# Performance work log

Hardware: AMD Instinct MI355X
Metric: run time of the kernel (lower is better)

The kernel has to match this reference:

```python
import jax, jax.numpy as jnp
import numpy as np

B, L, H, D = 4096, 256, 32, 2
LOG_PROB_FACTOR = 0.5

def setup_inputs() -> dict:
    key = jax.random.key(0)
    k0, k1, k2, k3 = jax.random.split(key, 4)
    x = jax.random.randint(k0, (B, L), 0, D)  # spin configs in {0,1}
    Wi = jax.random.normal(k1, (D, 4 * H), dtype=jnp.float32) * 0.1   # input kernel (no bias, flax LSTMCell)
    Wh = jax.random.normal(k2, (H, 4 * H), dtype=jnp.float32) * 0.1   # recurrent kernel
    bh = jnp.zeros((4 * H,), dtype=jnp.float32)                        # recurrent bias
    Wo = jax.random.normal(k3, (H, D), dtype=jnp.float32) * 0.1       # output Dense kernel
    bo = jnp.zeros((D,), dtype=jnp.float32)                            # output Dense bias
    return {"x": x, "Wi": Wi, "Wh": Wh, "bh": bh, "Wo": Wo, "bo": bo}

def reference(x, Wi, Wh, bh, Wo, bo):
    # one-hot of spin t-1 (zeros at t=0); log-prob is read out at spin t.
    x_oh = jax.nn.one_hot(x, D, dtype=Wi.dtype)      # [B, L, D]
    xs = jnp.swapaxes(x_oh, 0, 1)                    # [L, B, D] time-major for scan
    c0 = jnp.zeros((x.shape[0], H), Wi.dtype)
    h0 = jnp.zeros((x.shape[0], H), Wi.dtype)
    inp0 = jnp.zeros((x.shape[0], D), Wi.dtype)      # jnp.zeros(inputDim) initial input

    def step(carry, xt):
        c, h, inp = carry
        gates = inp @ Wi + h @ Wh + bh               # [B, 4H]
        i, f, g, o = jnp.split(gates, 4, axis=-1)    # flax LSTMCell gate order i,f,g,o
        c_new = jax.nn.sigmoid(f) * c + jax.nn.sigmoid(i) * jnp.tanh(g)
        h_new = jax.nn.sigmoid(o) * jnp.tanh(c_new)
        out = jax.nn.elu(h_new @ Wo + bo)            # Dense + actFun, [B, D]
        # log(sum(softmax(out) * onehot)) == gathered log_softmax (stable form)
        logp = jnp.sum(jax.nn.log_softmax(out, axis=-1) * xt, axis=-1)  # [B]
        return (c_new, h_new, xt), logp

    _, logps = jax.lax.scan(step, (c0, h0, inp0), xs)  # logps: [L, B]
    return LOG_PROB_FACTOR * jnp.sum(logps, axis=0)    # [B]
```

## Files before the change

kernel.cpp:

```cpp
#include <hip/hip_runtime.h>


typedef __attribute__((ext_vector_type(8))) short bf16x8;
typedef __attribute__((ext_vector_type(4))) float f32x4;

#define LOG2E 1.4426950408889634f
#define LN2   0.6931471805599453f

__device__ __forceinline__ float fexp2(float x) { return __builtin_amdgcn_exp2f(x); }
__device__ __forceinline__ float flog2(float x) { return __builtin_amdgcn_logf(x); }
__device__ __forceinline__ float frcp(float x)  { return __builtin_amdgcn_rcpf(x); }

__device__ __forceinline__ float fsig(float x)   { return frcp(1.f + fexp2(-LOG2E * x)); }
__device__ __forceinline__ float ftanh_(float x) { return 1.f - 2.f * frcp(fexp2(2.f * LOG2E * x) + 1.f); }
__device__ __forceinline__ float felu(float x)   { return x > 0.f ? x : fexp2(LOG2E * x) - 1.f; }

__device__ __forceinline__ unsigned short f2bf(float f) {
    unsigned u = __builtin_bit_cast(unsigned, f);
    u = (u + 0x7FFFu + ((u >> 16) & 1u)) >> 16;
    return (unsigned short)u;
}

constexpr int Bsz = 4096;

__global__ __launch_bounds__(512, 2) void lstm_r10(
    const int*   __restrict__ x,
    const float* __restrict__ Wi,
    const float* __restrict__ Wh,
    const float* __restrict__ bh,
    const float* __restrict__ Wo,
    const float* __restrict__ bo,
    float*       __restrict__ out)
{
    const int tid  = threadIdx.x;
    const int w    = tid >> 6;
    const int lane = tid & 63;
    const int m    = lane & 15;
    const int oct  = lane >> 4;
    const int rot  = w & 3;
    const int half = w >> 2;
    const int b0   = blockIdx.x * 16;

    __shared__ char   spinT[16][260];
    __shared__ float2 Sbuf[256][16];
    __shared__ short  hbuf[2][16][40];
    __shared__ float  red[8][16];

    {
        const int bl = tid >> 5;
        const int c8 = (tid & 31) * 8;
        const int4* src = reinterpret_cast<const int4*>(x + (b0 + bl) * 256 + c8);
        const int4 v0 = src[0], v1 = src[1];
        const int p0 = (v0.x & 1) | ((v0.y & 1) << 8) | ((v0.z & 1) << 16) | ((v0.w & 1) << 24);
        const int p1 = (v1.x & 1) | ((v1.y & 1) << 8) | ((v1.z & 1) << 16) | ((v1.w & 1) << 24);
        *reinterpret_cast<int*>(&spinT[bl][c8])     = p0;
        *reinterpret_cast<int*>(&spinT[bl][c8 + 4]) = p1;
    }

    bf16x8 wfrag[4];
#pragma unroll
    for (int q = 0; q < 4; ++q) {
        const float gs = (q == 2) ? 2.f * LOG2E : -LOG2E;
        const int colg = 32 * q + 16 * half + ((m + rot) & 15);
#pragma unroll
        for (int j = 0; j < 8; ++j)
            wfrag[q][j] = (short)f2bf(gs * Wh[(oct * 8 + j) * 128 + colg]);
    }
    bf16x8 wofragA;
#pragma unroll
    for (int j = 0; j < 8; ++j)
        wofragA[j] = (m < 2) ? (short)f2bf(Wo[(oct * 8 + j) * 2 + m]) : (short)0;

    const int ucell = 4 * oct + rot + 16 * half;
    float bv0[4], bvd[4];
#pragma unroll
    for (int q = 0; q < 4; ++q) {
        const float gs = (q == 2) ? 2.f * LOG2E : -LOG2E;
        const int c0 = 32 * q + ucell;
        bv0[q] = gs * (bh[c0] + Wi[c0]);
        bvd[q] = gs * (Wi[128 + c0] - Wi[c0]);
    }
    const float bo0 = bo[0], bo1 = bo[1];

    float c = fsig(bh[ucell]) * ftanh_(bh[64 + ucell]);
    hbuf[0][m][ucell] = (short)f2bf(fsig(bh[96 + ucell]) * ftanh_(c));
    __syncthreads();

    const f32x4 zero4 = { 0.f, 0.f, 0.f, 0.f };
    f32x4 ccq[4] = { zero4, zero4, zero4, zero4 };

    auto step = [&](const int t, const int rb, const int wb, const float spf) {
        const bf16x8 hfrag =
            *reinterpret_cast<const bf16x8*>(&hbuf[rb][m][8 * oct]);

#pragma unroll
        for (int q = 0; q < 4; ++q) ccq[q][0] = fmaf(spf, bvd[q], bv0[q]);

        f32x4 acc[4];
#pragma unroll
        for (int q = 0; q < 4; ++q)
            acc[q] = __builtin_amdgcn_mfma_f32_16x16x32_bf16(wfrag[q], hfrag, ccq[q], 0, 0, 0);

        if (((t - 1) & 7) == w) {
            const f32x4 hacc =
                __builtin_amdgcn_mfma_f32_16x16x32_bf16(wofragA, hfrag, zero4, 0, 0, 0);
            if (oct == 0) Sbuf[t - 1][m] = make_float2(hacc[0], hacc[1]);
        }

        {
            const float ei = fexp2(acc[0][0]), ef = fexp2(acc[1][0]);
            const float eg = fexp2(acc[2][0]), eo = fexp2(acc[3][0]);
            const float P = (1.f + ei) * (1.f + eg);
            const float Q = 1.f + ef;
            const float R = frcp(P * Q);
            const float gf  = P * R;
            const float igt = (eg - 1.f) * Q * R;
            c = fmaf(gf, c, igt);
            const float ec = fexp2(2.f * LOG2E * c);
            const float h  = (ec - 1.f) * frcp((1.f + eo) * (1.f + ec));
            hbuf[wb][m][ucell] = (short)f2bf(h);
        }
        __syncthreads();
    };

    unsigned sp2 = *reinterpret_cast<const unsigned short*>(&spinT[m][0]);
    for (int tb = 1; tb < 255; tb += 2) {
        const unsigned sp2n =
            *reinterpret_cast<const unsigned short*>(&spinT[m][tb + 1]);
        step(tb,     0, 1, (float)(sp2 & 0xFFu));
        step(tb + 1, 1, 0, (float)(sp2 >> 8));
        sp2 = sp2n;
    }
    step(255, 0, 1, (float)(sp2 & 0xFFu));

    if (w == 7) {
        const bf16x8 hfrag = *reinterpret_cast<const bf16x8*>(&hbuf[1][m][8 * oct]);
        const f32x4 hacc =
            __builtin_amdgcn_mfma_f32_16x16x32_bf16(wofragA, hfrag, zero4, 0, 0, 0);
        if (oct == 0) Sbuf[255][m] = make_float2(hacc[0], hacc[1]);
    }
    __syncthreads();

    float lp = 0.f;
    {
        const int t0 = (w * 4 + oct) * 8;
#pragma unroll
        for (int i = 0; i < 8; ++i) {
            const int t = t0 + i;
            const float2 sv = Sbuf[t][m];
            const int sp = spinT[m][t];
            const float o0 = felu(sv.x + bo0);
            const float o1 = felu(sv.y + bo1);
            const float mx = fmaxf(o0, o1), mn = fminf(o0, o1);
            const float lse = mx + LN2 * flog2(1.f + fexp2(LOG2E * (mn - mx)));
            lp += (sp ? o1 : o0) - lse;
        }
    }
    lp += __shfl_xor(lp, 16, 64);
    lp += __shfl_xor(lp, 32, 64);
    if (lane < 16) red[w][lane] = lp;
    __syncthreads();
    if (tid < 16) {
        float s = 0.f;
#pragma unroll
        for (int ww = 0; ww < 8; ++ww) s += red[ww][tid];
        out[b0 + tid] = 0.5f * s;
    }
}

extern "C" void kernel_launch(void* const* d_in, const int* in_sizes, int n_in,
                              void* d_out, int out_size, void* d_ws, size_t ws_size,
                              hipStream_t stream) {
    const int*   x  = (const int*)d_in[0];
    const float* Wi = (const float*)d_in[1];
    const float* Wh = (const float*)d_in[2];
    const float* bh = (const float*)d_in[3];
    const float* Wo = (const float*)d_in[4];
    const float* bo = (const float*)d_in[5];
    float* out = (float*)d_out;

    lstm_r10<<<dim3(Bsz / 16), dim3(512), 0, stream>>>(x, Wi, Wh, bh, Wo, bo, out);
}
```

Baseline: 136.9 us.

## Pack spins as bits, unroll recurrence by 32, keep cell state pre-scaled

Spins are packed into one bit each in shared memory instead of one byte, so a single 32-bit word feeds 32 time steps. The recurrence loop is fully unrolled in chunks of 32 with compile-time buffer indices and Sbuf slots. The cell state is carried pre-multiplied by 2*log2(e), removing one multiply from the critical chain per step. The loop now also runs one extra step that computes an unused hidden state, and a redundant first wfrag loop remains but is overwritten; the larger unrolled body could raise register pressure or code size.

```diff
diff --git a/kernel.cpp b/kernel.cpp
--- a/kernel.cpp
+++ b/kernel.cpp
@@ -4,15 +4,16 @@
 typedef __attribute__((ext_vector_type(8))) short bf16x8;
 typedef __attribute__((ext_vector_type(4))) float f32x4;
 
-#define LOG2E 1.4426950408889634f
-#define LN2   0.6931471805599453f
+#define LOG2E  1.4426950408889634f
+#define TWOL   2.8853900817779268f
+#define LN2    0.6931471805599453f
 
 __device__ __forceinline__ float fexp2(float x) { return __builtin_amdgcn_exp2f(x); }
 __device__ __forceinline__ float flog2(float x) { return __builtin_amdgcn_logf(x); }
 __device__ __forceinline__ float frcp(float x)  { return __builtin_amdgcn_rcpf(x); }
 
 __device__ __forceinline__ float fsig(float x)   { return frcp(1.f + fexp2(-LOG2E * x)); }
-__device__ __forceinline__ float ftanh_(float x) { return 1.f - 2.f * frcp(fexp2(2.f * LOG2E * x) + 1.f); }
+__device__ __forceinline__ float ftanh_(float x) { return 1.f - 2.f * frcp(fexp2(TWOL * x) + 1.f); }
 __device__ __forceinline__ float felu(float x)   { return x > 0.f ? x : fexp2(LOG2E * x) - 1.f; }
 
 __device__ __forceinline__ unsigned short f2bf(float f) {
@@ -23,7 +24,7 @@
 
 constexpr int Bsz = 4096;
 
-__global__ __launch_bounds__(512, 2) void lstm_r10(
+__global__ __launch_bounds__(512, 2) void lstm_r11(
     const int*   __restrict__ x,
     const float* __restrict__ Wi,
     const float* __restrict__ Wh,
@@ -41,26 +42,37 @@
     const int half = w >> 2;
     const int b0   = blockIdx.x * 16;
 
-    __shared__ char   spinT[16][260];
-    __shared__ float2 Sbuf[256][16];
-    __shared__ short  hbuf[2][16][40];
-    __shared__ float  red[8][16];
+    __shared__ unsigned spinbits[16][8];
+    __shared__ float2   Sbuf[256][16];
+    __shared__ short    hbuf[2][16][40];
+    __shared__ float    red[8][16];
 
     {
         const int bl = tid >> 5;
         const int c8 = (tid & 31) * 8;
         const int4* src = reinterpret_cast<const int4*>(x + (b0 + bl) * 256 + c8);
         const int4 v0 = src[0], v1 = src[1];
-        const int p0 = (v0.x & 1) | ((v0.y & 1) << 8) | ((v0.z & 1) << 16) | ((v0.w & 1) << 24);
-        const int p1 = (v1.x & 1) | ((v1.y & 1) << 8) | ((v1.z & 1) << 16) | ((v1.w & 1) << 24);
-        *reinterpret_cast<int*>(&spinT[bl][c8])     = p0;
-        *reinterpret_cast<int*>(&spinT[bl][c8 + 4]) = p1;
+        const unsigned bv =
+            (v0.x & 1) | ((v0.y & 1) << 1) | ((v0.z & 1) << 2) | ((v0.w & 1) << 3) |
+            ((v1.x & 1) << 4) | ((v1.y & 1) << 5) | ((v1.z & 1) << 6) | ((v1.w & 1) << 7);
+        reinterpret_cast<char*>(spinbits)[bl * 32 + (tid & 31)] = (char)bv;
     }
 
     bf16x8 wfrag[4];
 #pragma unroll
     for (int q = 0; q < 4; ++q) {
-        const float gs = (q == 2) ? 2.f * LOG2E : -LOG2E;
+        const float gs = (q == 2) ? TWOL * 0.5f * 2.f : -LOG2E;
+        const float gss = (q == 2) ? TWOL : -LOG2E;
+        (void)gs;
+        const int colg = 32 * q + 16 * half + ((m + rot) & 15);
+#pragma unroll
+        for (int j = 0; j < 8; ++j)
+            wfrag[q][j] = (short)f2bf(((q == 2) ? TWOL * 0.5f : -LOG2E) * 2.f * 0.5f * Wh[(oct * 8 + j) * 128 + colg] * ((q == 2) ? 2.f : 1.f) / ((q == 2) ? 2.f : 1.f) * ((q == 2) ? 2.f : 1.f));
+        (void)gss;
+    }
+#pragma unroll
+    for (int q = 0; q < 4; ++q) {
+        const float gs = (q == 2) ? (2.f * LOG2E) : -LOG2E;
         const int colg = 32 * q + 16 * half + ((m + rot) & 15);
 #pragma unroll
         for (int j = 0; j < 8; ++j)
@@ -75,80 +87,74 @@
     float bv0[4], bvd[4];
 #pragma unroll
     for (int q = 0; q < 4; ++q) {
-        const float gs = (q == 2) ? 2.f * LOG2E : -LOG2E;
+        const float gs = (q == 2) ? (2.f * LOG2E) : -LOG2E;
         const int c0 = 32 * q + ucell;
         bv0[q] = gs * (bh[c0] + Wi[c0]);
         bvd[q] = gs * (Wi[128 + c0] - Wi[c0]);
     }
     const float bo0 = bo[0], bo1 = bo[1];
 
-    float c = fsig(bh[ucell]) * ftanh_(bh[64 + ucell]);
-    hbuf[0][m][ucell] = (short)f2bf(fsig(bh[96 + ucell]) * ftanh_(c));
+    float cp = TWOL * (fsig(bh[ucell]) * ftanh_(bh[64 + ucell]));
+    hbuf[0][m][ucell] = (short)f2bf(fsig(bh[96 + ucell]) * ftanh_(cp * (1.f / TWOL)));
     __syncthreads();
 
     const f32x4 zero4 = { 0.f, 0.f, 0.f, 0.f };
     f32x4 ccq[4] = { zero4, zero4, zero4, zero4 };
 
-    auto step = [&](const int t, const int rb, const int wb, const float spf) {
-        const bf16x8 hfrag =
-            *reinterpret_cast<const bf16x8*>(&hbuf[rb][m][8 * oct]);
+    unsigned cur = spinbits[m][0];
+    for (int k = 0; k < 8; ++k) {
+        const int tb = 32 * k + 1;
+        const unsigned nxt = spinbits[m][k < 7 ? k + 1 : 7];
+#pragma unroll
+        for (int i = 0; i < 32; ++i) {
+            const int rb = i & 1, wb = rb ^ 1;
+            const float spf = (float)((cur >> i) & 1u);
+
+            const bf16x8 hfrag =
+                *reinterpret_cast<const bf16x8*>(&hbuf[rb][m][8 * oct]);
 
 #pragma unroll
-        for (int q = 0; q < 4; ++q) ccq[q][0] = fmaf(spf, bvd[q], bv0[q]);
+            for (int q = 0; q < 4; ++q) ccq[q][0] = fmaf(spf, bvd[q], bv0[q]);
 
-        f32x4 acc[4];
+            f32x4 acc[4];
 #pragma unroll
-        for (int q = 0; q < 4; ++q)
-            acc[q] = __builtin_amdgcn_mfma_f32_16x16x32_bf16(wfrag[q], hfrag, ccq[q], 0, 0, 0);
+            for (int q = 0; q < 4; ++q)
+                acc[q] = __builtin_amdgcn_mfma_f32_16x16x32_bf16(wfrag[q], hfrag, ccq[q], 0, 0, 0);
 
-        if (((t - 1) & 7) == w) {
-            const f32x4 hacc =
-                __builtin_amdgcn_mfma_f32_16x16x32_bf16(wofragA, hfrag, zero4, 0, 0, 0);
-            if (oct == 0) Sbuf[t - 1][m] = make_float2(hacc[0], hacc[1]);
+            if ((i & 7) == w) {
+                const f32x4 hacc =
+                    __builtin_amdgcn_mfma_f32_16x16x32_bf16(wofragA, hfrag, zero4, 0, 0, 0);
+                if (oct == 0) Sbuf[tb - 1 + i][m] = make_float2(hacc[0], hacc[1]);
+            }
+
+            {
+                const float ei = fexp2(acc[0][0]), ef = fexp2(acc[1][0]);
+                const float eg = fexp2(acc[2][0]), eo = fexp2(acc[3][0]);
+                const float P  = (1.f + ei) * (1.f + eg);
+                const float Q  = 1.f + ef;
+                const float E  = fmaf(eg, TWOL, -TWOL);
+                const float R  = frcp(P * Q);
+                const float gf   = P * R;
+                const float igtp = E * Q * R;
+                cp = fmaf(gf, cp, igtp);
+                const float ec = fexp2(cp);
+                const float h  = (ec - 1.f) * frcp((1.f + eo) * (1.f + ec));
+                hbuf[wb][m][ucell] = (short)f2bf(h);
+            }
+            __syncthreads();
         }
-
-        {
-            const float ei = fexp2(acc[0][0]), ef = fexp2(acc[1][0]);
-            const float eg = fexp2(acc[2][0]), eo = fexp2(acc[3][0]);
-            const float P = (1.f + ei) * (1.f + eg);
-            const float Q = 1.f + ef;
-            const float R = frcp(P * Q);
-            const float gf  = P * R;
-            const float igt = (eg - 1.f) * Q * R;
-            c = fmaf(gf, c, igt);
-            const float ec = fexp2(2.f * LOG2E * c);
-            const float h  = (ec - 1.f) * frcp((1.f + eo) * (1.f + ec));
-            hbuf[wb][m][ucell] = (short)f2bf(h);
-        }
-        __syncthreads();
-    };
-
-    unsigned sp2 = *reinterpret_cast<const unsigned short*>(&spinT[m][0]);
-    for (int tb = 1; tb < 255; tb += 2) {
-        const unsigned sp2n =
-            *reinterpret_cast<const unsigned short*>(&spinT[m][tb + 1]);
-        step(tb,     0, 1, (float)(sp2 & 0xFFu));
-        step(tb + 1, 1, 0, (float)(sp2 >> 8));
-        sp2 = sp2n;
+        cur = nxt;
     }
-    step(255, 0, 1, (float)(sp2 & 0xFFu));
-
-    if (w == 7) {
-        const bf16x8 hfrag = *reinterpret_cast<const bf16x8*>(&hbuf[1][m][8 * oct]);
-        const f32x4 hacc =
-            __builtin_amdgcn_mfma_f32_16x16x32_bf16(wofragA, hfrag, zero4, 0, 0, 0);
-        if (oct == 0) Sbuf[255][m] = make_float2(hacc[0], hacc[1]);
-    }
-    __syncthreads();
 
     float lp = 0.f;
     {
-        const int t0 = (w * 4 + oct) * 8;
+        const unsigned sw = spinbits[m][w] >> (8 * oct);
+        const int t0 = w * 32 + oct * 8;
 #pragma unroll
         for (int i = 0; i < 8; ++i) {
             const int t = t0 + i;
             const float2 sv = Sbuf[t][m];
-            const int sp = spinT[m][t];
+            const int sp = (sw >> i) & 1u;
             const float o0 = felu(sv.x + bo0);
             const float o1 = felu(sv.y + bo1);
             const float mx = fmaxf(o0, o1), mn = fminf(o0, o1);
@@ -179,5 +185,5 @@
     const float* bo = (const float*)d_in[5];
     float* out = (float*)d_out;
 
-    lstm_r10<<<dim3(Bsz / 16), dim3(512), 0, stream>>>(x, Wi, Wh, bh, Wo, bo, out);
+    lstm_r11<<<dim3(Bsz / 16), dim3(512), 0, stream>>>(x, Wi, Wh, bh, Wo, bo, out);
 }
```

Result: no change. 137.0 us (+0.0%).
